# Kernel tuning notes

Measured on AMD Instinct MI355X. Metric: run time of the kernel, lower is better.

Reference implementation:

```python
import jax, jax.numpy as jnp
import numpy as np
from jax import lax

NEG = -10000.0
B, L, D = 256, 1024, 126  # batch, doc_len, d_output (tags); padded tagset T = D + 2


def setup_inputs() -> dict:
    key = jax.random.key(0)
    k1, k2, k3, k4 = jax.random.split(key, 4)
    x = jax.random.normal(k1, (B, L, D), dtype=jnp.float32)
    transitions = jax.random.normal(k2, (D + 2, D + 2), dtype=jnp.float32)
    x_len = jax.random.randint(k3, (B,), 1, L + 1, dtype=jnp.int32)
    x_mask = (jnp.arange(L)[None, :] < x_len[:, None]).astype(jnp.float32)
    true_tag = jax.random.randint(k4, (B, L), 0, D, dtype=jnp.int32)
    return {"x": x, "transitions": transitions, "x_mask": x_mask,
            "x_len": x_len, "true_tag": true_tag}


def _loglikelihood(x, transitions, x_mask, x_len, true_tag):
    b, l, d = x.shape
    T = transitions.shape[0]
    START, STOP = T - 2, T - 1
    # pad emissions with two impossible tags (START/STOP)
    logits = jnp.concatenate([x, jnp.full((b, l, 2), NEG, x.dtype)], axis=2)  # [B,L,T]

    # ---- partition function (forward algorithm, log-sum-exp scan) ----
    alpha0 = jnp.full((b, T), NEG, x.dtype).at[:, START].set(0.0)

    def step(alpha, inp):
        logit, m = inp  # [B,T], [B]
        # mat[b,i,j] = trans[i,j] + alpha[b,j] + logit[b,i]
        mat = transitions[None, :, :] + alpha[:, None, :] + logit[:, :, None]
        new = jax.nn.logsumexp(mat, axis=2)  # [B,T]
        m = m[:, None]
        return m * new + (1.0 - m) * alpha, None

    alpha, _ = lax.scan(step, alpha0, (jnp.swapaxes(logits, 0, 1), x_mask.T))
    partition = jax.nn.logsumexp(alpha + transitions[STOP][None, :], axis=1)  # [B]

    # ---- gold sequence score ----
    tag = true_tag.astype(jnp.int32)
    emission = jnp.take_along_axis(logits, tag[:, :, None], axis=2)[:, :, 0]
    emission = jnp.sum(emission * x_mask, axis=1)  # [B]

    tran = transitions[tag[:, 0], START]  # START -> first tag
    pair = transitions[tag[:, 1:], tag[:, :-1]] * x_mask[:, 1:]  # trans[next, prev]
    tran = tran + jnp.sum(pair, axis=1)
    last_tag = jnp.take_along_axis(tag, (x_len.astype(jnp.int32) - 1)[:, None], axis=1)[:, 0]
    tran = tran + transitions[STOP, last_tag]

    return tran + emission - partition  # [B]


def reference(x, transitions, x_mask, x_len, true_tag):
    return _loglikelihood(x, transitions, x_mask, x_len, true_tag)
```

## Files before the change

### kernel.cpp

```cpp
#include <hip/hip_runtime.h>


#define LOG2E   1.4426950408889634f
#define LN2     0.6931471805599453f

constexpr int Bc = 256, Lc = 1024, Dc = 126, Tc = 128;
constexpr int CH = 16, CHF = CH * Dc;
constexpr int NCH = Lc / CH;

#if __has_builtin(__builtin_amdgcn_exp2f)
#define FEXP2(x) __builtin_amdgcn_exp2f(x)
#else
#define FEXP2(x) exp2f(x)
#endif
#if __has_builtin(__builtin_amdgcn_logf)
#define FLOG2(x) __builtin_amdgcn_logf(x)
#else
#define FLOG2(x) log2f(x)
#endif

#if __has_builtin(__builtin_amdgcn_mov_dpp)
#define DPPF(x, ctrl) __int_as_float(__builtin_amdgcn_mov_dpp(__float_as_int(x), (ctrl), 0xF, 0xF, true))
#define ROR1(x) DPPF(x, 0x121)
#define ROR2(x) DPPF(x, 0x122)
#define ROR4(x) DPPF(x, 0x124)
#define ROR8(x) DPPF(x, 0x128)
#else
#define ROR1(x) __shfl_xor((x), 1, 64)
#define ROR2(x) __shfl_xor((x), 2, 64)
#define ROR4(x) __shfl_xor((x), 4, 64)
#define ROR8(x) __shfl_xor((x), 8, 64)
#endif

#define STEP_BARRIER() asm volatile("s_waitcnt lgkmcnt(0)\n\ts_barrier" ::: "memory")

__global__ __launch_bounds__(512, 1) void crf_fwd_kernel(
    const float* __restrict__ x,
    const float* __restrict__ trans,
    const int*   __restrict__ x_len,
    const int*   __restrict__ tag,
    float*       __restrict__ out)
{
    __shared__ __align__(16) float E[2][Tc];
    __shared__ __align__(16) float Lbuf[2][CHF];
    __shared__ float red[12];

    const int b   = blockIdx.x;
    const int tid = threadIdx.x;
    const int w   = tid >> 6;
    const int l6  = tid & 63;
    const int o   = l6 & 15;
    const int jg  = (w << 2) | (l6 >> 4);
    const int len = x_len[b];

    const float* xb = x   + (size_t)b * Lc * Dc;
    const int*   tb = tag + (size_t)b * Lc;

    const int sw   = 4 * (o >> 2);
    const int i0   = (o << 3) ^ sw;
    const int i1   = ((o << 3) + 4) ^ sw;
    const int jw   = 4 * jg + (o & 3);
    const int widx = jw ^ (4 * (jw >> 5));
    const int jr   = (jw < Dc) ? jw : 0;

    float treg[4][8];
#pragma unroll
    for (int g = 0; g < 4; ++g) {
        const float4* tp = reinterpret_cast<const float4*>(trans + (4*jg + g) * Tc + 8*o);
        float4 t0 = tp[0], t1 = tp[1];
        treg[g][0] = FEXP2(t0.x * LOG2E); treg[g][1] = FEXP2(t0.y * LOG2E);
        treg[g][2] = FEXP2(t0.z * LOG2E); treg[g][3] = FEXP2(t0.w * LOG2E);
        treg[g][4] = FEXP2(t1.x * LOG2E); treg[g][5] = FEXP2(t1.y * LOG2E);
        treg[g][6] = FEXP2(t1.z * LOG2E); treg[g][7] = FEXP2(t1.w * LOG2E);
    }

    {
        float4 q0 = make_float4(0.f, 0.f, 0.f, 0.f);
        if (tid < CHF / 4) q0 = *reinterpret_cast<const float4*>(xb + 4 * tid);
        if (tid < Tc) E[0][tid ^ (4 * (tid >> 5))] = (tid == Tc - 2) ? 1.0f : 0.0f;
        if (tid < CHF / 4) *reinterpret_cast<float4*>(&Lbuf[0][4 * tid]) = q0;
    }
    __syncthreads();

    float P    = (jw < Dc) ? FEXP2(Lbuf[0][jr] * LOG2E) : 0.0f;
    int   Mint = 0;
    float4 stq = make_float4(0.f, 0.f, 0.f, 0.f);

    for (int l = 0; l < len; ++l) {
        const int p   = l & 1;
        const int sub = l & (CH - 1);
        const int cb  = (l >> 4) & 1;

        if (sub == 0) {
            const int c1 = (l >> 4) + 1;
            if (c1 < NCH && tid < CHF / 4)
                stq = *reinterpret_cast<const float4*>(xb + (size_t)c1 * CHF + 4 * tid);
        } else if (sub == 8) {
            const int c1 = (l >> 4) + 1;
            if (c1 < NCH && tid < CHF / 4)
                *reinterpret_cast<float4*>(&Lbuf[cb ^ 1][4 * tid]) = stq;
        }

        const float* Ep = E[p];
        float4 ea  = *reinterpret_cast<const float4*>(Ep + i0);
        float4 eb4 = *reinterpret_cast<const float4*>(Ep + i1);

        const int ln = (l + 1 < len) ? (l + 1) : l;
        const float lv = Lbuf[(ln >> 4) & 1][(ln & (CH - 1)) * Dc + jr];

        float a0 = treg[0][0] * ea.x, a1 = treg[1][0] * ea.x,
              a2 = treg[2][0] * ea.x, a3 = treg[3][0] * ea.x;
        a0 = fmaf(treg[0][1], ea.y, a0);  a1 = fmaf(treg[1][1], ea.y, a1);
        a2 = fmaf(treg[2][1], ea.y, a2);  a3 = fmaf(treg[3][1], ea.y, a3);
        a0 = fmaf(treg[0][2], ea.z, a0);  a1 = fmaf(treg[1][2], ea.z, a1);
        a2 = fmaf(treg[2][2], ea.z, a2);  a3 = fmaf(treg[3][2], ea.z, a3);
        a0 = fmaf(treg[0][3], ea.w, a0);  a1 = fmaf(treg[1][3], ea.w, a1);
        a2 = fmaf(treg[2][3], ea.w, a2);  a3 = fmaf(treg[3][3], ea.w, a3);
        a0 = fmaf(treg[0][4], eb4.x, a0); a1 = fmaf(treg[1][4], eb4.x, a1);
        a2 = fmaf(treg[2][4], eb4.x, a2); a3 = fmaf(treg[3][4], eb4.x, a3);
        a0 = fmaf(treg[0][5], eb4.y, a0); a1 = fmaf(treg[1][5], eb4.y, a1);
        a2 = fmaf(treg[2][5], eb4.y, a2); a3 = fmaf(treg[3][5], eb4.y, a3);
        a0 = fmaf(treg[0][6], eb4.z, a0); a1 = fmaf(treg[1][6], eb4.z, a1);
        a2 = fmaf(treg[2][6], eb4.z, a2); a3 = fmaf(treg[3][6], eb4.z, a3);
        a0 = fmaf(treg[0][7], eb4.w, a0); a1 = fmaf(treg[1][7], eb4.w, a1);
        a2 = fmaf(treg[2][7], eb4.w, a2); a3 = fmaf(treg[3][7], eb4.w, a3);

        a0 += ROR1(a0); a1 += ROR1(a1); a2 += ROR1(a2); a3 += ROR1(a3);
        a0 += ROR2(a0); a1 += ROR2(a1); a2 += ROR2(a2); a3 += ROR2(a3);
        a0 += ROR4(a0); a1 += ROR4(a1); a2 += ROR4(a2); a3 += ROR4(a3);
        a0 += ROR8(a0); a1 += ROR8(a1); a2 += ROR8(a2); a3 += ROR8(a3);

        float R;
        if ((l & 3) == 3) {
            float mx = fmaxf(ea.z, eb4.z);
            mx = fmaxf(mx, ROR1(mx)); mx = fmaxf(mx, ROR2(mx));
            mx = fmaxf(mx, ROR4(mx)); mx = fmaxf(mx, ROR8(mx));
            int ebq = (__float_as_int(mx) >> 23) & 0xFF;
            R = __int_as_float((254 - ebq) << 23);
            Mint += ebq - 127;
        } else {
            R = 1.0f;
        }

        float sel = a0;
        sel = (o == 1) ? a1 : sel;
        sel = (o == 2) ? a2 : sel;
        sel = (o == 3) ? a3 : sel;
        float eout = sel * P * R;
        if (o < 4) E[p ^ 1][widx] = eout;

        P = (jw < Dc) ? FEXP2(lv * LOG2E) : 0.0f;

        STEP_BARRIER();
    }
    const int pf = len & 1;

    float acc = 0.f;
    for (int l = tid; l < len; l += 512) {
        int   tg = tb[l];
        float tr = (l == 0) ? trans[tg * Tc + (Tc - 2)]
                            : trans[tg * Tc + tb[l - 1]];
        acc += xb[(size_t)l * Dc + tg] + tr;
    }
#pragma unroll
    for (int off = 1; off < 64; off <<= 1)
        acc += __shfl_xor(acc, off, 64);
    if (l6 == 0) red[w] = acc;

    if (w == 0) {
        int k0i = l6, k1i = 64 + l6;
        float p0 = FEXP2(trans[(Tc-1) * Tc + k0i] * LOG2E) * E[pf][k0i ^ (4 * (k0i >> 5))];
        float p1 = FEXP2(trans[(Tc-1) * Tc + k1i] * LOG2E) * E[pf][k1i ^ (4 * (k1i >> 5))];
        float ps = p0 + p1;
#pragma unroll
        for (int off = 1; off < 64; off <<= 1)
            ps += __shfl_xor(ps, off, 64);
        if (l6 == 0) red[8] = LN2 * ((float)Mint + FLOG2(ps));
    }
    __syncthreads();

    if (tid == 0) {
        float sc = trans[(Tc-1) * Tc + tb[len - 1]];
#pragma unroll
        for (int i = 0; i < 8; ++i) sc += red[i];
        out[b] = sc - red[8];
    }
}

extern "C" void kernel_launch(void* const* d_in, const int* in_sizes, int n_in,
                              void* d_out, int out_size, void* d_ws, size_t ws_size,
                              hipStream_t stream) {
    const float* x     = (const float*)d_in[0];
    const float* trans = (const float*)d_in[1];
    const int*   x_len = (const int*)d_in[3];
    const int*   tag   = (const int*)d_in[4];
    float*       out   = (float*)d_out;

    crf_fwd_kernel<<<Bc, 512, 0, stream>>>(x, trans, x_len, tag, out);
}
```

Measured before the change: 536.7 us.

## Pack two batch sequences per 1024-thread block sharing one step barrier

```diff
diff --git a/kernel.cpp b/kernel.cpp
--- a/kernel.cpp
+++ b/kernel.cpp
@@ -34,24 +34,27 @@
 
 #define STEP_BARRIER() asm volatile("s_waitcnt lgkmcnt(0)\n\ts_barrier" ::: "memory")
 
-__global__ __launch_bounds__(512, 1) void crf_fwd_kernel(
+__global__ __launch_bounds__(1024, 1) void crf_fwd_kernel(
     const float* __restrict__ x,
     const float* __restrict__ trans,
     const int*   __restrict__ x_len,
     const int*   __restrict__ tag,
     float*       __restrict__ out)
 {
-    __shared__ __align__(16) float E[2][Tc];
-    __shared__ __align__(16) float Lbuf[2][CHF];
-    __shared__ float red[12];
-
-    const int b   = blockIdx.x;
-    const int tid = threadIdx.x;
-    const int w   = tid >> 6;
-    const int l6  = tid & 63;
-    const int o   = l6 & 15;
-    const int jg  = (w << 2) | (l6 >> 4);
-    const int len = x_len[b];
+    __shared__ __align__(16) float E[2][2][Tc];
+    __shared__ __align__(16) float Lbuf[2][2][CHF];
+    __shared__ float red[2][12];
+    __shared__ int   lens[2];
+
+    const int tid  = threadIdx.x;
+    const int half = tid >> 9;
+    const int tA   = tid & 511;
+    const int b    = (blockIdx.x << 1) | half;
+    const int w    = tA >> 6;
+    const int l6   = tid & 63;
+    const int o    = l6 & 15;
+    const int jg   = (w << 2) | (l6 >> 4);
+    const int len  = x_len[b];
 
     const float* xb = x   + (size_t)b * Lc * Dc;
     const int*   tb = tag + (size_t)b * Lc;
@@ -76,87 +79,90 @@
 
     {
         float4 q0 = make_float4(0.f, 0.f, 0.f, 0.f);
-        if (tid < CHF / 4) q0 = *reinterpret_cast<const float4*>(xb + 4 * tid);
-        if (tid < Tc) E[0][tid ^ (4 * (tid >> 5))] = (tid == Tc - 2) ? 1.0f : 0.0f;
-        if (tid < CHF / 4) *reinterpret_cast<float4*>(&Lbuf[0][4 * tid]) = q0;
+        if (tA < CHF / 4) q0 = *reinterpret_cast<const float4*>(xb + 4 * tA);
+        if (tA < Tc) E[half][0][tA ^ (4 * (tA >> 5))] = (tA == Tc - 2) ? 1.0f : 0.0f;
+        if (tA < CHF / 4) *reinterpret_cast<float4*>(&Lbuf[half][0][4 * tA]) = q0;
+        if (tA == 0) lens[half] = len;
     }
     __syncthreads();
-
-    float P    = (jw < Dc) ? FEXP2(Lbuf[0][jr] * LOG2E) : 0.0f;
+    const int lenmax = max(lens[0], lens[1]);
+
+    float P    = (jw < Dc) ? FEXP2(Lbuf[half][0][jr] * LOG2E) : 0.0f;
     int   Mint = 0;
     float4 stq = make_float4(0.f, 0.f, 0.f, 0.f);
 
-    for (int l = 0; l < len; ++l) {
-        const int p   = l & 1;
-        const int sub = l & (CH - 1);
-        const int cb  = (l >> 4) & 1;
-
-        if (sub == 0) {
-            const int c1 = (l >> 4) + 1;
-            if (c1 < NCH && tid < CHF / 4)
-                stq = *reinterpret_cast<const float4*>(xb + (size_t)c1 * CHF + 4 * tid);
-        } else if (sub == 8) {
-            const int c1 = (l >> 4) + 1;
-            if (c1 < NCH && tid < CHF / 4)
-                *reinterpret_cast<float4*>(&Lbuf[cb ^ 1][4 * tid]) = stq;
+    for (int l = 0; l < lenmax; ++l) {
+        if (l < len) {
+            const int p   = l & 1;
+            const int sub = l & (CH - 1);
+            const int cb  = (l >> 4) & 1;
+
+            if (sub == 0) {
+                const int c1 = (l >> 4) + 1;
+                if (c1 < NCH && tA < CHF / 4)
+                    stq = *reinterpret_cast<const float4*>(xb + (size_t)c1 * CHF + 4 * tA);
+            } else if (sub == 8) {
+                const int c1 = (l >> 4) + 1;
+                if (c1 < NCH && tA < CHF / 4)
+                    *reinterpret_cast<float4*>(&Lbuf[half][cb ^ 1][4 * tA]) = stq;
+            }
+
+            const float* Ep = E[half][p];
+            float4 ea  = *reinterpret_cast<const float4*>(Ep + i0);
+            float4 eb4 = *reinterpret_cast<const float4*>(Ep + i1);
+
+            const int ln = (l + 1 < len) ? (l + 1) : l;
+            const float lv = Lbuf[half][(ln >> 4) & 1][(ln & (CH - 1)) * Dc + jr];
+
+            float a0 = treg[0][0] * ea.x, a1 = treg[1][0] * ea.x,
+                  a2 = treg[2][0] * ea.x, a3 = treg[3][0] * ea.x;
+            a0 = fmaf(treg[0][1], ea.y, a0);  a1 = fmaf(treg[1][1], ea.y, a1);
+            a2 = fmaf(treg[2][1], ea.y, a2);  a3 = fmaf(treg[3][1], ea.y, a3);
+            a0 = fmaf(treg[0][2], ea.z, a0);  a1 = fmaf(treg[1][2], ea.z, a1);
+            a2 = fmaf(treg[2][2], ea.z, a2);  a3 = fmaf(treg[3][2], ea.z, a3);
+            a0 = fmaf(treg[0][3], ea.w, a0);  a1 = fmaf(treg[1][3], ea.w, a1);
+            a2 = fmaf(treg[2][3], ea.w, a2);  a3 = fmaf(treg[3][3], ea.w, a3);
+            a0 = fmaf(treg[0][4], eb4.x, a0); a1 = fmaf(treg[1][4], eb4.x, a1);
+            a2 = fmaf(treg[2][4], eb4.x, a2); a3 = fmaf(treg[3][4], eb4.x, a3);
+            a0 = fmaf(treg[0][5], eb4.y, a0); a1 = fmaf(treg[1][5], eb4.y, a1);
+            a2 = fmaf(treg[2][5], eb4.y, a2); a3 = fmaf(treg[3][5], eb4.y, a3);
+            a0 = fmaf(treg[0][6], eb4.z, a0); a1 = fmaf(treg[1][6], eb4.z, a1);
+            a2 = fmaf(treg[2][6], eb4.z, a2); a3 = fmaf(treg[3][6], eb4.z, a3);
+            a0 = fmaf(treg[0][7], eb4.w, a0); a1 = fmaf(treg[1][7], eb4.w, a1);
+            a2 = fmaf(treg[2][7], eb4.w, a2); a3 = fmaf(treg[3][7], eb4.w, a3);
+
+            a0 += ROR1(a0); a1 += ROR1(a1); a2 += ROR1(a2); a3 += ROR1(a3);
+            a0 += ROR2(a0); a1 += ROR2(a1); a2 += ROR2(a2); a3 += ROR2(a3);
+            a0 += ROR4(a0); a1 += ROR4(a1); a2 += ROR4(a2); a3 += ROR4(a3);
+            a0 += ROR8(a0); a1 += ROR8(a1); a2 += ROR8(a2); a3 += ROR8(a3);
+
+            float R;
+            if ((l & 3) == 3) {
+                float mx = fmaxf(ea.z, eb4.z);
+                mx = fmaxf(mx, ROR1(mx)); mx = fmaxf(mx, ROR2(mx));
+                mx = fmaxf(mx, ROR4(mx)); mx = fmaxf(mx, ROR8(mx));
+                int ebq = (__float_as_int(mx) >> 23) & 0xFF;
+                R = __int_as_float((254 - ebq) << 23);
+                Mint += ebq - 127;
+            } else {
+                R = 1.0f;
+            }
+
+            float sel = a0;
+            sel = (o == 1) ? a1 : sel;
+            sel = (o == 2) ? a2 : sel;
+            sel = (o == 3) ? a3 : sel;
+            float eout = sel * P * R;
+            if (o < 4) E[half][p ^ 1][widx] = eout;
+
+            P = (jw < Dc) ? FEXP2(lv * LOG2E) : 0.0f;
         }
-
-        const float* Ep = E[p];
-        float4 ea  = *reinterpret_cast<const float4*>(Ep + i0);
-        float4 eb4 = *reinterpret_cast<const float4*>(Ep + i1);
-
-        const int ln = (l + 1 < len) ? (l + 1) : l;
-        const float lv = Lbuf[(ln >> 4) & 1][(ln & (CH - 1)) * Dc + jr];
-
-        float a0 = treg[0][0] * ea.x, a1 = treg[1][0] * ea.x,
-              a2 = treg[2][0] * ea.x, a3 = treg[3][0] * ea.x;
-        a0 = fmaf(treg[0][1], ea.y, a0);  a1 = fmaf(treg[1][1], ea.y, a1);
-        a2 = fmaf(treg[2][1], ea.y, a2);  a3 = fmaf(treg[3][1], ea.y, a3);
-        a0 = fmaf(treg[0][2], ea.z, a0);  a1 = fmaf(treg[1][2], ea.z, a1);
-        a2 = fmaf(treg[2][2], ea.z, a2);  a3 = fmaf(treg[3][2], ea.z, a3);
-        a0 = fmaf(treg[0][3], ea.w, a0);  a1 = fmaf(treg[1][3], ea.w, a1);
-        a2 = fmaf(treg[2][3], ea.w, a2);  a3 = fmaf(treg[3][3], ea.w, a3);
-        a0 = fmaf(treg[0][4], eb4.x, a0); a1 = fmaf(treg[1][4], eb4.x, a1);
-        a2 = fmaf(treg[2][4], eb4.x, a2); a3 = fmaf(treg[3][4], eb4.x, a3);
-        a0 = fmaf(treg[0][5], eb4.y, a0); a1 = fmaf(treg[1][5], eb4.y, a1);
-        a2 = fmaf(treg[2][5], eb4.y, a2); a3 = fmaf(treg[3][5], eb4.y, a3);
-        a0 = fmaf(treg[0][6], eb4.z, a0); a1 = fmaf(treg[1][6], eb4.z, a1);
-        a2 = fmaf(treg[2][6], eb4.z, a2); a3 = fmaf(treg[3][6], eb4.z, a3);
-        a0 = fmaf(treg[0][7], eb4.w, a0); a1 = fmaf(treg[1][7], eb4.w, a1);
-        a2 = fmaf(treg[2][7], eb4.w, a2); a3 = fmaf(treg[3][7], eb4.w, a3);
-
-        a0 += ROR1(a0); a1 += ROR1(a1); a2 += ROR1(a2); a3 += ROR1(a3);
-        a0 += ROR2(a0); a1 += ROR2(a1); a2 += ROR2(a2); a3 += ROR2(a3);
-        a0 += ROR4(a0); a1 += ROR4(a1); a2 += ROR4(a2); a3 += ROR4(a3);
-        a0 += ROR8(a0); a1 += ROR8(a1); a2 += ROR8(a2); a3 += ROR8(a3);
-
-        float R;
-        if ((l & 3) == 3) {
-            float mx = fmaxf(ea.z, eb4.z);
-            mx = fmaxf(mx, ROR1(mx)); mx = fmaxf(mx, ROR2(mx));
-            mx = fmaxf(mx, ROR4(mx)); mx = fmaxf(mx, ROR8(mx));
-            int ebq = (__float_as_int(mx) >> 23) & 0xFF;
-            R = __int_as_float((254 - ebq) << 23);
-            Mint += ebq - 127;
-        } else {
-            R = 1.0f;
-        }
-
-        float sel = a0;
-        sel = (o == 1) ? a1 : sel;
-        sel = (o == 2) ? a2 : sel;
-        sel = (o == 3) ? a3 : sel;
-        float eout = sel * P * R;
-        if (o < 4) E[p ^ 1][widx] = eout;
-
-        P = (jw < Dc) ? FEXP2(lv * LOG2E) : 0.0f;
-
         STEP_BARRIER();
     }
     const int pf = len & 1;
 
     float acc = 0.f;
-    for (int l = tid; l < len; l += 512) {
+    for (int l = tA; l < len; l += 512) {
         int   tg = tb[l];
         float tr = (l == 0) ? trans[tg * Tc + (Tc - 2)]
                             : trans[tg * Tc + tb[l - 1]];
@@ -165,25 +171,25 @@
 #pragma unroll
     for (int off = 1; off < 64; off <<= 1)
         acc += __shfl_xor(acc, off, 64);
-    if (l6 == 0) red[w] = acc;
+    if (l6 == 0) red[half][w] = acc;
 
     if (w == 0) {
         int k0i = l6, k1i = 64 + l6;
-        float p0 = FEXP2(trans[(Tc-1) * Tc + k0i] * LOG2E) * E[pf][k0i ^ (4 * (k0i >> 5))];
-        float p1 = FEXP2(trans[(Tc-1) * Tc + k1i] * LOG2E) * E[pf][k1i ^ (4 * (k1i >> 5))];
+        float p0 = FEXP2(trans[(Tc-1) * Tc + k0i] * LOG2E) * E[half][pf][k0i ^ (4 * (k0i >> 5))];
+        float p1 = FEXP2(trans[(Tc-1) * Tc + k1i] * LOG2E) * E[half][pf][k1i ^ (4 * (k1i >> 5))];
         float ps = p0 + p1;
 #pragma unroll
         for (int off = 1; off < 64; off <<= 1)
             ps += __shfl_xor(ps, off, 64);
-        if (l6 == 0) red[8] = LN2 * ((float)Mint + FLOG2(ps));
+        if (l6 == 0) red[half][8] = LN2 * ((float)Mint + FLOG2(ps));
     }
     __syncthreads();
 
-    if (tid == 0) {
+    if (tA == 0) {
         float sc = trans[(Tc-1) * Tc + tb[len - 1]];
 #pragma unroll
-        for (int i = 0; i < 8; ++i) sc += red[i];
-        out[b] = sc - red[8];
+        for (int i = 0; i < 8; ++i) sc += red[half][i];
+        out[b] = sc - red[half][8];
     }
 }
 
@@ -196,5 +202,5 @@
     const int*   tag   = (const int*)d_in[4];
     float*       out   = (float*)d_out;
 
-    crf_fwd_kernel<<<Bc, 512, 0, stream>>>(x, trans, x_len, tag, out);
+    crf_fwd_kernel<<<Bc / 2, 1024, 0, stream>>>(x, trans, x_len, tag, out);
 }
```

New measurement: 796.0 us. 1.48x slower.

## Halve block to 256 threads with 16-wide k per lane and 8-lane reductions

Applied to the files above, without the earlier changes.

```diff
diff --git a/kernel.cpp b/kernel.cpp
--- a/kernel.cpp
+++ b/kernel.cpp
@@ -21,20 +21,24 @@
 
 #if __has_builtin(__builtin_amdgcn_mov_dpp)
 #define DPPF(x, ctrl) __int_as_float(__builtin_amdgcn_mov_dpp(__float_as_int(x), (ctrl), 0xF, 0xF, true))
-#define ROR1(x) DPPF(x, 0x121)
-#define ROR2(x) DPPF(x, 0x122)
-#define ROR4(x) DPPF(x, 0x124)
-#define ROR8(x) DPPF(x, 0x128)
+#define QX1(x)  DPPF(x, 0xB1)
+#define QX2(x)  DPPF(x, 0x4E)
+#define HMIR(x) DPPF(x, 0x141)
 #else
-#define ROR1(x) __shfl_xor((x), 1, 64)
-#define ROR2(x) __shfl_xor((x), 2, 64)
-#define ROR4(x) __shfl_xor((x), 4, 64)
-#define ROR8(x) __shfl_xor((x), 8, 64)
+#define QX1(x)  __shfl_xor((x), 1, 64)
+#define QX2(x)  __shfl_xor((x), 2, 64)
+#define HMIR(x) __shfl_xor((x), 4, 64)
 #endif
 
 #define STEP_BARRIER() asm volatile("s_waitcnt lgkmcnt(0)\n\ts_barrier" ::: "memory")
 
-__global__ __launch_bounds__(512, 1) void crf_fwd_kernel(
+__device__ __forceinline__ int Fmap(int k) {
+    int q = k >> 2;
+    q ^= (q >> 3) & 3;
+    return 4 * q + (k & 3);
+}
+
+__global__ __launch_bounds__(256, 1) void crf_fwd_kernel(
     const float* __restrict__ x,
     const float* __restrict__ trans,
     const int*   __restrict__ x_len,
@@ -49,42 +53,52 @@
     const int tid = threadIdx.x;
     const int w   = tid >> 6;
     const int l6  = tid & 63;
-    const int o   = l6 & 15;
-    const int jg  = (w << 2) | (l6 >> 4);
+    const int kg  = l6 & 7;
+    const int jg  = (w << 3) | (l6 >> 3);
     const int len = x_len[b];
 
     const float* xb = x   + (size_t)b * Lc * Dc;
     const int*   tb = tag + (size_t)b * Lc;
 
-    const int sw   = 4 * (o >> 2);
-    const int i0   = (o << 3) ^ sw;
-    const int i1   = ((o << 3) + 4) ^ sw;
-    const int jw   = 4 * jg + (o & 3);
-    const int widx = jw ^ (4 * (jw >> 5));
-    const int jr   = (jw < Dc) ? jw : 0;
-
-    float treg[4][8];
+    int f0, f1, f2, f3;
+    {
+        int q0 = 4 * kg + 0; q0 ^= (q0 >> 3) & 3; f0 = 4 * q0;
+        int q1 = 4 * kg + 1; q1 ^= (q1 >> 3) & 3; f1 = 4 * q1;
+        int q2 = 4 * kg + 2; q2 ^= (q2 >> 3) & 3; f2 = 4 * q2;
+        int q3 = 4 * kg + 3; q3 ^= (q3 >> 3) & 3; f3 = 4 * q3;
+    }
+    const int  jw   = 4 * jg + (kg & 3);
+    const int  widx = Fmap(jw);
+    const int  jr   = (jw < Dc) ? jw : 0;
+    const bool wr   = (kg < 4);
+
+    float treg[4][16];
 #pragma unroll
     for (int g = 0; g < 4; ++g) {
-        const float4* tp = reinterpret_cast<const float4*>(trans + (4*jg + g) * Tc + 8*o);
-        float4 t0 = tp[0], t1 = tp[1];
-        treg[g][0] = FEXP2(t0.x * LOG2E); treg[g][1] = FEXP2(t0.y * LOG2E);
-        treg[g][2] = FEXP2(t0.z * LOG2E); treg[g][3] = FEXP2(t0.w * LOG2E);
-        treg[g][4] = FEXP2(t1.x * LOG2E); treg[g][5] = FEXP2(t1.y * LOG2E);
-        treg[g][6] = FEXP2(t1.z * LOG2E); treg[g][7] = FEXP2(t1.w * LOG2E);
+        const float4* tp = reinterpret_cast<const float4*>(trans + (4*jg + g) * Tc + 16*kg);
+#pragma unroll
+        for (int c4 = 0; c4 < 4; ++c4) {
+            float4 t4 = tp[c4];
+            treg[g][4*c4+0] = FEXP2(t4.x * LOG2E);
+            treg[g][4*c4+1] = FEXP2(t4.y * LOG2E);
+            treg[g][4*c4+2] = FEXP2(t4.z * LOG2E);
+            treg[g][4*c4+3] = FEXP2(t4.w * LOG2E);
+        }
     }
 
     {
-        float4 q0 = make_float4(0.f, 0.f, 0.f, 0.f);
-        if (tid < CHF / 4) q0 = *reinterpret_cast<const float4*>(xb + 4 * tid);
-        if (tid < Tc) E[0][tid ^ (4 * (tid >> 5))] = (tid == Tc - 2) ? 1.0f : 0.0f;
-        if (tid < CHF / 4) *reinterpret_cast<float4*>(&Lbuf[0][4 * tid]) = q0;
+        float4 q0 = *reinterpret_cast<const float4*>(xb + 4 * tid);
+        float4 q1 = make_float4(0.f, 0.f, 0.f, 0.f);
+        if (tid < (CHF/4 - 256)) q1 = *reinterpret_cast<const float4*>(xb + 1024 + 4 * tid);
+        if (tid < Tc) E[0][Fmap(tid)] = (tid == Tc - 2) ? 1.0f : 0.0f;
+        *reinterpret_cast<float4*>(&Lbuf[0][4 * tid]) = q0;
+        if (tid < (CHF/4 - 256)) *reinterpret_cast<float4*>(&Lbuf[0][1024 + 4 * tid]) = q1;
     }
     __syncthreads();
 
     float P    = (jw < Dc) ? FEXP2(Lbuf[0][jr] * LOG2E) : 0.0f;
     int   Mint = 0;
-    float4 stq = make_float4(0.f, 0.f, 0.f, 0.f);
+    float4 s0q = make_float4(0.f,0.f,0.f,0.f), s1q = make_float4(0.f,0.f,0.f,0.f);
 
     for (int l = 0; l < len; ++l) {
         const int p   = l & 1;
@@ -93,48 +107,59 @@
 
         if (sub == 0) {
             const int c1 = (l >> 4) + 1;
-            if (c1 < NCH && tid < CHF / 4)
-                stq = *reinterpret_cast<const float4*>(xb + (size_t)c1 * CHF + 4 * tid);
+            if (c1 < NCH) {
+                const float* src = xb + (size_t)c1 * CHF;
+                s0q = *reinterpret_cast<const float4*>(src + 4 * tid);
+                if (tid < (CHF/4 - 256))
+                    s1q = *reinterpret_cast<const float4*>(src + 1024 + 4 * tid);
+            }
         } else if (sub == 8) {
             const int c1 = (l >> 4) + 1;
-            if (c1 < NCH && tid < CHF / 4)
-                *reinterpret_cast<float4*>(&Lbuf[cb ^ 1][4 * tid]) = stq;
+            if (c1 < NCH) {
+                *reinterpret_cast<float4*>(&Lbuf[cb ^ 1][4 * tid]) = s0q;
+                if (tid < (CHF/4 - 256))
+                    *reinterpret_cast<float4*>(&Lbuf[cb ^ 1][1024 + 4 * tid]) = s1q;
+            }
         }
 
         const float* Ep = E[p];
-        float4 ea  = *reinterpret_cast<const float4*>(Ep + i0);
-        float4 eb4 = *reinterpret_cast<const float4*>(Ep + i1);
+        float4 e0 = *reinterpret_cast<const float4*>(Ep + f0);
+        float4 e1 = *reinterpret_cast<const float4*>(Ep + f1);
+        float4 e2 = *reinterpret_cast<const float4*>(Ep + f2);
+        float4 e3 = *reinterpret_cast<const float4*>(Ep + f3);
 
         const int ln = (l + 1 < len) ? (l + 1) : l;
         const float lv = Lbuf[(ln >> 4) & 1][(ln & (CH - 1)) * Dc + jr];
 
-        float a0 = treg[0][0] * ea.x, a1 = treg[1][0] * ea.x,
-              a2 = treg[2][0] * ea.x, a3 = treg[3][0] * ea.x;
-        a0 = fmaf(treg[0][1], ea.y, a0);  a1 = fmaf(treg[1][1], ea.y, a1);
-        a2 = fmaf(treg[2][1], ea.y, a2);  a3 = fmaf(treg[3][1], ea.y, a3);
-        a0 = fmaf(treg[0][2], ea.z, a0);  a1 = fmaf(treg[1][2], ea.z, a1);
-        a2 = fmaf(treg[2][2], ea.z, a2);  a3 = fmaf(treg[3][2], ea.z, a3);
-        a0 = fmaf(treg[0][3], ea.w, a0);  a1 = fmaf(treg[1][3], ea.w, a1);
-        a2 = fmaf(treg[2][3], ea.w, a2);  a3 = fmaf(treg[3][3], ea.w, a3);
-        a0 = fmaf(treg[0][4], eb4.x, a0); a1 = fmaf(treg[1][4], eb4.x, a1);
-        a2 = fmaf(treg[2][4], eb4.x, a2); a3 = fmaf(treg[3][4], eb4.x, a3);
-        a0 = fmaf(treg[0][5], eb4.y, a0); a1 = fmaf(treg[1][5], eb4.y, a1);
-        a2 = fmaf(treg[2][5], eb4.y, a2); a3 = fmaf(treg[3][5], eb4.y, a3);
-        a0 = fmaf(treg[0][6], eb4.z, a0); a1 = fmaf(treg[1][6], eb4.z, a1);
-        a2 = fmaf(treg[2][6], eb4.z, a2); a3 = fmaf(treg[3][6], eb4.z, a3);
-        a0 = fmaf(treg[0][7], eb4.w, a0); a1 = fmaf(treg[1][7], eb4.w, a1);
-        a2 = fmaf(treg[2][7], eb4.w, a2); a3 = fmaf(treg[3][7], eb4.w, a3);
-
-        a0 += ROR1(a0); a1 += ROR1(a1); a2 += ROR1(a2); a3 += ROR1(a3);
-        a0 += ROR2(a0); a1 += ROR2(a1); a2 += ROR2(a2); a3 += ROR2(a3);
-        a0 += ROR4(a0); a1 += ROR4(a1); a2 += ROR4(a2); a3 += ROR4(a3);
-        a0 += ROR8(a0); a1 += ROR8(a1); a2 += ROR8(a2); a3 += ROR8(a3);
+        float a0, a1, a2, a3;
+        {
+            float l0 = treg[0][0]*e0.x, l1 = treg[1][0]*e0.x, l2 = treg[2][0]*e0.x, l3 = treg[3][0]*e0.x;
+            float h0 = treg[0][8]*e2.x, h1 = treg[1][8]*e2.x, h2 = treg[2][8]*e2.x, h3 = treg[3][8]*e2.x;
+            l0=fmaf(treg[0][1],e0.y,l0); l1=fmaf(treg[1][1],e0.y,l1); l2=fmaf(treg[2][1],e0.y,l2); l3=fmaf(treg[3][1],e0.y,l3);
+            h0=fmaf(treg[0][9],e2.y,h0); h1=fmaf(treg[1][9],e2.y,h1); h2=fmaf(treg[2][9],e2.y,h2); h3=fmaf(treg[3][9],e2.y,h3);
+            l0=fmaf(treg[0][2],e0.z,l0); l1=fmaf(treg[1][2],e0.z,l1); l2=fmaf(treg[2][2],e0.z,l2); l3=fmaf(treg[3][2],e0.z,l3);
+            h0=fmaf(treg[0][10],e2.z,h0); h1=fmaf(treg[1][10],e2.z,h1); h2=fmaf(treg[2][10],e2.z,h2); h3=fmaf(treg[3][10],e2.z,h3);
+            l0=fmaf(treg[0][3],e0.w,l0); l1=fmaf(treg[1][3],e0.w,l1); l2=fmaf(treg[2][3],e0.w,l2); l3=fmaf(treg[3][3],e0.w,l3);
+            h0=fmaf(treg[0][11],e2.w,h0); h1=fmaf(treg[1][11],e2.w,h1); h2=fmaf(treg[2][11],e2.w,h2); h3=fmaf(treg[3][11],e2.w,h3);
+            l0=fmaf(treg[0][4],e1.x,l0); l1=fmaf(treg[1][4],e1.x,l1); l2=fmaf(treg[2][4],e1.x,l2); l3=fmaf(treg[3][4],e1.x,l3);
+            h0=fmaf(treg[0][12],e3.x,h0); h1=fmaf(treg[1][12],e3.x,h1); h2=fmaf(treg[2][12],e3.x,h2); h3=fmaf(treg[3][12],e3.x,h3);
+            l0=fmaf(treg[0][5],e1.y,l0); l1=fmaf(treg[1][5],e1.y,l1); l2=fmaf(treg[2][5],e1.y,l2); l3=fmaf(treg[3][5],e1.y,l3);
+            h0=fmaf(treg[0][13],e3.y,h0); h1=fmaf(treg[1][13],e3.y,h1); h2=fmaf(treg[2][13],e3.y,h2); h3=fmaf(treg[3][13],e3.y,h3);
+            l0=fmaf(treg[0][6],e1.z,l0); l1=fmaf(treg[1][6],e1.z,l1); l2=fmaf(treg[2][6],e1.z,l2); l3=fmaf(treg[3][6],e1.z,l3);
+            h0=fmaf(treg[0][14],e3.z,h0); h1=fmaf(treg[1][14],e3.z,h1); h2=fmaf(treg[2][14],e3.z,h2); h3=fmaf(treg[3][14],e3.z,h3);
+            l0=fmaf(treg[0][7],e1.w,l0); l1=fmaf(treg[1][7],e1.w,l1); l2=fmaf(treg[2][7],e1.w,l2); l3=fmaf(treg[3][7],e1.w,l3);
+            h0=fmaf(treg[0][15],e3.w,h0); h1=fmaf(treg[1][15],e3.w,h1); h2=fmaf(treg[2][15],e3.w,h2); h3=fmaf(treg[3][15],e3.w,h3);
+            a0 = l0 + h0; a1 = l1 + h1; a2 = l2 + h2; a3 = l3 + h3;
+        }
+
+        a0 += QX1(a0);  a1 += QX1(a1);  a2 += QX1(a2);  a3 += QX1(a3);
+        a0 += QX2(a0);  a1 += QX2(a1);  a2 += QX2(a2);  a3 += QX2(a3);
+        a0 += HMIR(a0); a1 += HMIR(a1); a2 += HMIR(a2); a3 += HMIR(a3);
 
         float R;
         if ((l & 3) == 3) {
-            float mx = fmaxf(ea.z, eb4.z);
-            mx = fmaxf(mx, ROR1(mx)); mx = fmaxf(mx, ROR2(mx));
-            mx = fmaxf(mx, ROR4(mx)); mx = fmaxf(mx, ROR8(mx));
+            float mx = fmaxf(fmaxf(e0.z, e1.z), fmaxf(e2.z, e3.z));
+            mx = fmaxf(mx, QX1(mx)); mx = fmaxf(mx, QX2(mx)); mx = fmaxf(mx, HMIR(mx));
             int ebq = (__float_as_int(mx) >> 23) & 0xFF;
             R = __int_as_float((254 - ebq) << 23);
             Mint += ebq - 127;
@@ -143,11 +168,11 @@
         }
 
         float sel = a0;
-        sel = (o == 1) ? a1 : sel;
-        sel = (o == 2) ? a2 : sel;
-        sel = (o == 3) ? a3 : sel;
+        sel = (kg == 1) ? a1 : sel;
+        sel = (kg == 2) ? a2 : sel;
+        sel = (kg == 3) ? a3 : sel;
         float eout = sel * P * R;
-        if (o < 4) E[p ^ 1][widx] = eout;
+        if (wr) E[p ^ 1][widx] = eout;
 
         P = (jw < Dc) ? FEXP2(lv * LOG2E) : 0.0f;
 
@@ -156,7 +181,7 @@
     const int pf = len & 1;
 
     float acc = 0.f;
-    for (int l = tid; l < len; l += 512) {
+    for (int l = tid; l < len; l += 256) {
         int   tg = tb[l];
         float tr = (l == 0) ? trans[tg * Tc + (Tc - 2)]
                             : trans[tg * Tc + tb[l - 1]];
@@ -169,8 +194,8 @@
 
     if (w == 0) {
         int k0i = l6, k1i = 64 + l6;
-        float p0 = FEXP2(trans[(Tc-1) * Tc + k0i] * LOG2E) * E[pf][k0i ^ (4 * (k0i >> 5))];
-        float p1 = FEXP2(trans[(Tc-1) * Tc + k1i] * LOG2E) * E[pf][k1i ^ (4 * (k1i >> 5))];
+        float p0 = FEXP2(trans[(Tc-1) * Tc + k0i] * LOG2E) * E[pf][Fmap(k0i)];
+        float p1 = FEXP2(trans[(Tc-1) * Tc + k1i] * LOG2E) * E[pf][Fmap(k1i)];
         float ps = p0 + p1;
 #pragma unroll
         for (int off = 1; off < 64; off <<= 1)
@@ -182,7 +207,7 @@
     if (tid == 0) {
         float sc = trans[(Tc-1) * Tc + tb[len - 1]];
 #pragma unroll
-        for (int i = 0; i < 8; ++i) sc += red[i];
+        for (int i = 0; i < 4; ++i) sc += red[i];
         out[b] = sc - red[8];
     }
 }
@@ -196,5 +221,5 @@
     const int*   tag   = (const int*)d_in[4];
     float*       out   = (float*)d_out;
 
-    crf_fwd_kernel<<<Bc, 512, 0, stream>>>(x, trans, x_len, tag, out);
+    crf_fwd_kernel<<<Bc, 256, 0, stream>>>(x, trans, x_len, tag, out);
 }
```

After: 586.4 us. 1.09x slower.

## Replace LDS emission staging with per-thread register prefetch and unroll by four

Applied to the files above, without the earlier changes.

```diff
diff --git a/kernel.cpp b/kernel.cpp
--- a/kernel.cpp
+++ b/kernel.cpp
@@ -1,12 +1,13 @@
 #include <hip/hip_runtime.h>
 
 
-#define LOG2E   1.4426950408889634f
-#define LN2     0.6931471805599453f
+typedef float v2f __attribute__((ext_vector_type(2)));
+
+#define NEGV  (-10000.0f)
+#define LOG2E 1.4426950408889634f
+#define LN2   0.6931471805599453f
 
 constexpr int Bc = 256, Lc = 1024, Dc = 126, Tc = 128;
-constexpr int CH = 16, CHF = CH * Dc;
-constexpr int NCH = Lc / CH;
 
 #if __has_builtin(__builtin_amdgcn_exp2f)
 #define FEXP2(x) __builtin_amdgcn_exp2f(x)
@@ -34,6 +35,9 @@
 
 #define STEP_BARRIER() asm volatile("s_waitcnt lgkmcnt(0)\n\ts_barrier" ::: "memory")
 
+__device__ __forceinline__ int SIG(int q) { return q ^ (q >> 3); }
+__device__ __forceinline__ int Fmap(int k) { return 4 * SIG(k >> 2) + (k & 3); }
+
 __global__ __launch_bounds__(512, 1) void crf_fwd_kernel(
     const float* __restrict__ x,
     const float* __restrict__ trans,
@@ -42,7 +46,6 @@
     float*       __restrict__ out)
 {
     __shared__ __align__(16) float E[2][Tc];
-    __shared__ __align__(16) float Lbuf[2][CHF];
     __shared__ float red[12];
 
     const int b   = blockIdx.x;
@@ -56,12 +59,10 @@
     const float* xb = x   + (size_t)b * Lc * Dc;
     const int*   tb = tag + (size_t)b * Lc;
 
-    const int sw   = 4 * (o >> 2);
-    const int i0   = (o << 3) ^ sw;
-    const int i1   = ((o << 3) + 4) ^ sw;
-    const int jw   = 4 * jg + (o & 3);
-    const int widx = jw ^ (4 * (jw >> 5));
-    const int jr   = (jw < Dc) ? jw : 0;
+    const int  f0 = 4 * SIG(2 * o);
+    const int  f1 = 4 * SIG(2 * o + 1);
+    const int  wq = 4 * SIG(jg);
+    const bool hiBad = (jg == 31);
 
     float treg[4][8];
 #pragma unroll
@@ -74,85 +75,83 @@
         treg[g][6] = FEXP2(t1.z * LOG2E); treg[g][7] = FEXP2(t1.w * LOG2E);
     }
 
-    {
-        float4 q0 = make_float4(0.f, 0.f, 0.f, 0.f);
-        if (tid < CHF / 4) q0 = *reinterpret_cast<const float4*>(xb + 4 * tid);
-        if (tid < Tc) E[0][tid ^ (4 * (tid >> 5))] = (tid == Tc - 2) ? 1.0f : 0.0f;
-        if (tid < CHF / 4) *reinterpret_cast<float4*>(&Lbuf[0][4 * tid]) = q0;
-    }
+    if (tid < Tc) E[0][Fmap(tid)] = (tid == Tc - 2) ? 1.0f : 0.0f;
     __syncthreads();
 
-    float P    = (jw < Dc) ? FEXP2(Lbuf[0][jr] * LOG2E) : 0.0f;
-    int   Mint = 0;
-    float4 stq = make_float4(0.f, 0.f, 0.f, 0.f);
+#define LOADP(LS, A, B2) {                                              \
+        int _s = (LS); if (_s > len - 1) _s = len - 1;                  \
+        const float* _r = xb + (size_t)_s * Dc + 4 * jg;                \
+        A  = *reinterpret_cast<const v2f*>(_r);                         \
+        B2 = hiBad ? (v2f){NEGV, NEGV}                                  \
+                   : *reinterpret_cast<const v2f*>(_r + 2); }
 
-    for (int l = 0; l < len; ++l) {
-        const int p   = l & 1;
-        const int sub = l & (CH - 1);
-        const int cb  = (l >> 4) & 1;
+    v2f Pa, Pb;
+    {
+        v2f a, b2; LOADP(0, a, b2);
+        Pa = (v2f){FEXP2(a.x * LOG2E),  FEXP2(a.y * LOG2E)};
+        Pb = (v2f){FEXP2(b2.x * LOG2E), FEXP2(b2.y * LOG2E)};
+    }
+    v2f pA0, pB0, pA1, pB1, pA2, pB2, pA3, pB3;
+    LOADP(1, pA1, pB1); LOADP(2, pA2, pB2); LOADP(3, pA3, pB3);
+    pA0 = pA1; pB0 = pB1;
 
-        if (sub == 0) {
-            const int c1 = (l >> 4) + 1;
-            if (c1 < NCH && tid < CHF / 4)
-                stq = *reinterpret_cast<const float4*>(xb + (size_t)c1 * CHF + 4 * tid);
-        } else if (sub == 8) {
-            const int c1 = (l >> 4) + 1;
-            if (c1 < NCH && tid < CHF / 4)
-                *reinterpret_cast<float4*>(&Lbuf[cb ^ 1][4 * tid]) = stq;
-        }
+    int Mint = 0;
+    const int len4 = (len + 3) & ~3;
 
-        const float* Ep = E[p];
-        float4 ea  = *reinterpret_cast<const float4*>(Ep + i0);
-        float4 eb4 = *reinterpret_cast<const float4*>(Ep + i1);
+#define BODY(C, PA_LD, PB_LD, PA_NX, PB_NX) {                                   \
+        const int  l   = l4 + (C);                                              \
+        const bool act = l < len;                 \
+        const int  p   = (C) & 1;                                               \
+        LOADP(l + 4, PA_LD, PB_LD);           \
+        const float* Ep = E[p];                                                 \
+        float4 ea = *reinterpret_cast<const float4*>(Ep + f0);                  \
+        float4 eb = *reinterpret_cast<const float4*>(Ep + f1);                  \
+        float a0 = treg[0][0]*ea.x, a1 = treg[1][0]*ea.x,                       \
+              a2 = treg[2][0]*ea.x, a3 = treg[3][0]*ea.x;                       \
+        a0=fmaf(treg[0][1],ea.y,a0); a1=fmaf(treg[1][1],ea.y,a1);               \
+        a2=fmaf(treg[2][1],ea.y,a2); a3=fmaf(treg[3][1],ea.y,a3);               \
+        a0=fmaf(treg[0][2],ea.z,a0); a1=fmaf(treg[1][2],ea.z,a1);               \
+        a2=fmaf(treg[2][2],ea.z,a2); a3=fmaf(treg[3][2],ea.z,a3);               \
+        a0=fmaf(treg[0][3],ea.w,a0); a1=fmaf(treg[1][3],ea.w,a1);               \
+        a2=fmaf(treg[2][3],ea.w,a2); a3=fmaf(treg[3][3],ea.w,a3);               \
+        a0=fmaf(treg[0][4],eb.x,a0); a1=fmaf(treg[1][4],eb.x,a1);               \
+        a2=fmaf(treg[2][4],eb.x,a2); a3=fmaf(treg[3][4],eb.x,a3);               \
+        a0=fmaf(treg[0][5],eb.y,a0); a1=fmaf(treg[1][5],eb.y,a1);               \
+        a2=fmaf(treg[2][5],eb.y,a2); a3=fmaf(treg[3][5],eb.y,a3);               \
+        a0=fmaf(treg[0][6],eb.z,a0); a1=fmaf(treg[1][6],eb.z,a1);               \
+        a2=fmaf(treg[2][6],eb.z,a2); a3=fmaf(treg[3][6],eb.z,a3);               \
+        a0=fmaf(treg[0][7],eb.w,a0); a1=fmaf(treg[1][7],eb.w,a1);               \
+        a2=fmaf(treg[2][7],eb.w,a2); a3=fmaf(treg[3][7],eb.w,a3);               \
+        a0 += ROR1(a0); a1 += ROR1(a1); a2 += ROR1(a2); a3 += ROR1(a3);         \
+        a0 += ROR2(a0); a1 += ROR2(a1); a2 += ROR2(a2); a3 += ROR2(a3);         \
+        a0 += ROR4(a0); a1 += ROR4(a1); a2 += ROR4(a2); a3 += ROR4(a3);         \
+        a0 += ROR8(a0); a1 += ROR8(a1); a2 += ROR8(a2); a3 += ROR8(a3);         \
+        float R = 1.0f;                                                         \
+        if ((C) == 3 && act) {               \
+            float mx = fmaxf(ea.z, eb.z);                                       \
+            mx = fmaxf(mx, ROR1(mx)); mx = fmaxf(mx, ROR2(mx));                 \
+            mx = fmaxf(mx, ROR4(mx)); mx = fmaxf(mx, ROR8(mx));                 \
+            int ebq = (__float_as_int(mx) >> 23) & 0xFF;                        \
+            R = __int_as_float((254 - ebq) << 23);                              \
+            Mint += ebq - 127;                                                  \
+        }                                                                       \
+        if (act && o == 0)                 \
+            *reinterpret_cast<float4*>(&E[p ^ 1][wq]) =                         \
+                make_float4(a0 * Pa.x * R, a1 * Pa.y * R,                       \
+                            a2 * Pb.x * R, a3 * Pb.y * R);                      \
+        Pa = (v2f){FEXP2(PA_NX.x * LOG2E), FEXP2(PA_NX.y * LOG2E)};             \
+        Pb = (v2f){FEXP2(PB_NX.x * LOG2E), FEXP2(PB_NX.y * LOG2E)};             \
+        STEP_BARRIER();                                                         \
+    }
 
-        const int ln = (l + 1 < len) ? (l + 1) : l;
-        const float lv = Lbuf[(ln >> 4) & 1][(ln & (CH - 1)) * Dc + jr];
-
-        float a0 = treg[0][0] * ea.x, a1 = treg[1][0] * ea.x,
-              a2 = treg[2][0] * ea.x, a3 = treg[3][0] * ea.x;
-        a0 = fmaf(treg[0][1], ea.y, a0);  a1 = fmaf(treg[1][1], ea.y, a1);
-        a2 = fmaf(treg[2][1], ea.y, a2);  a3 = fmaf(treg[3][1], ea.y, a3);
-        a0 = fmaf(treg[0][2], ea.z, a0);  a1 = fmaf(treg[1][2], ea.z, a1);
-        a2 = fmaf(treg[2][2], ea.z, a2);  a3 = fmaf(treg[3][2], ea.z, a3);
-        a0 = fmaf(treg[0][3], ea.w, a0);  a1 = fmaf(treg[1][3], ea.w, a1);
-        a2 = fmaf(treg[2][3], ea.w, a2);  a3 = fmaf(treg[3][3], ea.w, a3);
-        a0 = fmaf(treg[0][4], eb4.x, a0); a1 = fmaf(treg[1][4], eb4.x, a1);
-        a2 = fmaf(treg[2][4], eb4.x, a2); a3 = fmaf(treg[3][4], eb4.x, a3);
-        a0 = fmaf(treg[0][5], eb4.y, a0); a1 = fmaf(treg[1][5], eb4.y, a1);
-        a2 = fmaf(treg[2][5], eb4.y, a2); a3 = fmaf(treg[3][5], eb4.y, a3);
-        a0 = fmaf(treg[0][6], eb4.z, a0); a1 = fmaf(treg[1][6], eb4.z, a1);
-        a2 = fmaf(treg[2][6], eb4.z, a2); a3 = fmaf(treg[3][6], eb4.z, a3);
-        a0 = fmaf(treg[0][7], eb4.w, a0); a1 = fmaf(treg[1][7], eb4.w, a1);
-        a2 = fmaf(treg[2][7], eb4.w, a2); a3 = fmaf(treg[3][7], eb4.w, a3);
-
-        a0 += ROR1(a0); a1 += ROR1(a1); a2 += ROR1(a2); a3 += ROR1(a3);
-        a0 += ROR2(a0); a1 += ROR2(a1); a2 += ROR2(a2); a3 += ROR2(a3);
-        a0 += ROR4(a0); a1 += ROR4(a1); a2 += ROR4(a2); a3 += ROR4(a3);
-        a0 += ROR8(a0); a1 += ROR8(a1); a2 += ROR8(a2); a3 += ROR8(a3);
-
-        float R;
-        if ((l & 3) == 3) {
-            float mx = fmaxf(ea.z, eb4.z);
-            mx = fmaxf(mx, ROR1(mx)); mx = fmaxf(mx, ROR2(mx));
-            mx = fmaxf(mx, ROR4(mx)); mx = fmaxf(mx, ROR8(mx));
-            int ebq = (__float_as_int(mx) >> 23) & 0xFF;
-            R = __int_as_float((254 - ebq) << 23);
-            Mint += ebq - 127;
-        } else {
-            R = 1.0f;
-        }
-
-        float sel = a0;
-        sel = (o == 1) ? a1 : sel;
-        sel = (o == 2) ? a2 : sel;
-        sel = (o == 3) ? a3 : sel;
-        float eout = sel * P * R;
-        if (o < 4) E[p ^ 1][widx] = eout;
-
-        P = (jw < Dc) ? FEXP2(lv * LOG2E) : 0.0f;
-
-        STEP_BARRIER();
+    for (int l4 = 0; l4 < len4; l4 += 4) {
+        BODY(0, pA0, pB0, pA1, pB1)
+        BODY(1, pA1, pB1, pA2, pB2)
+        BODY(2, pA2, pB2, pA3, pB3)
+        BODY(3, pA3, pB3, pA0, pB0)
     }
+#undef BODY
+#undef LOADP
     const int pf = len & 1;
 
     float acc = 0.f;
@@ -169,8 +168,8 @@
 
     if (w == 0) {
         int k0i = l6, k1i = 64 + l6;
-        float p0 = FEXP2(trans[(Tc-1) * Tc + k0i] * LOG2E) * E[pf][k0i ^ (4 * (k0i >> 5))];
-        float p1 = FEXP2(trans[(Tc-1) * Tc + k1i] * LOG2E) * E[pf][k1i ^ (4 * (k1i >> 5))];
+        float p0 = FEXP2(trans[(Tc-1) * Tc + k0i] * LOG2E) * E[pf][Fmap(k0i)];
+        float p1 = FEXP2(trans[(Tc-1) * Tc + k1i] * LOG2E) * E[pf][Fmap(k1i)];
         float ps = p0 + p1;
 #pragma unroll
         for (int off = 1; off < 64; off <<= 1)
```

Result: no change. 545.4 us (+1.6%).
